# Kernel optimization log

Measured on AMD Instinct MI355X. Metric: run time of the kernel, lower is better.

The kernel has to match this reference:

```python
import jax, jax.numpy as jnp
import numpy as np


def _row_distance(a, b):
    # pairwise cosine similarity between rows of a [N,D] and b [K,D] -> [N,K]
    an = a / (jnp.linalg.norm(a, axis=1, keepdims=True) + 1e-12)
    bn = b / (jnp.linalg.norm(b, axis=1, keepdims=True) + 1e-12)
    return an @ bn.T


def _nearest_context(feature, context):
    sim = _row_distance(feature, context)          # [B, K]
    # distances = -sim; argmin(distances) == argmax(sim)
    min_ind = jnp.argmax(sim, axis=1)              # [B]
    onehot = jax.nn.one_hot(min_ind, context.shape[0], dtype=feature.dtype)  # [B, K]
    rslt = onehot @ jax.lax.stop_gradient(context)  # [B, E] codebook gather
    return rslt, onehot


@jax.custom_vjp
def _vq(feature, context):
    return _nearest_context(feature, context)[0]


def _vq_fwd(feature, context):
    value, ind = _nearest_context(feature, context)
    return value, ind


def _vq_bwd(ind, d_value):
    # straight-through to feature; scatter grads into codebook rows
    return (d_value, ind.T @ d_value)


_vq.defvjp(_vq_fwd, _vq_bwd)


def setup_inputs() -> dict:
    key = jax.random.key(0)
    ks = jax.random.split(key, 6)
    B, FEAT, MID, EMB, K = 8192, 4096, 512, 256, 512
    return {
        "x": jax.random.normal(ks[0], (B, FEAT), dtype=jnp.float32),
        "enc_w1": jax.random.normal(ks[1], (FEAT, MID), dtype=jnp.float32) * 0.02,
        "enc_b1": jnp.zeros((MID,), dtype=jnp.float32),
        "enc_w2": jax.random.normal(ks[2], (MID, EMB), dtype=jnp.float32) * 0.02,
        "enc_b2": jnp.zeros((EMB,), dtype=jnp.float32),
        "emb": jax.random.normal(ks[3], (K, EMB), dtype=jnp.float32) * 0.01,
        "dec_w1": jax.random.normal(ks[4], (EMB, MID), dtype=jnp.float32) * 0.02,
        "dec_b1": jnp.zeros((MID,), dtype=jnp.float32),
        "dec_w2": jax.random.normal(ks[5], (MID, FEAT), dtype=jnp.float32) * 0.02,
        "dec_b2": jnp.zeros((FEAT,), dtype=jnp.float32),
    }


def reference(x, enc_w1, enc_b1, enc_w2, enc_b2, emb, dec_w1, dec_b1, dec_w2, dec_b2):
    # encoder (stand-in for MultiContextEncoder with out_size=(middle_dim, emb_dim))
    h = jax.nn.relu(x @ enc_w1 + enc_b1)           # [B, MID]
    encoded = h @ enc_w2 + enc_b2                  # [B, EMB]
    # vector quantization with straight-through gradient
    vq_feat = _vq(encoded, emb)                    # [B, EMB]
    _, context_ind = _nearest_context(encoded, emb)  # [B, K] one-hot
    # decoder: Dense(middle_dim, relu) -> Dense(feat_dim, relu)
    d = jax.nn.relu(vq_feat @ dec_w1 + dec_b1)     # [B, MID]
    decoded = jax.nn.relu(d @ dec_w2 + dec_b2)     # [B, FEAT]
    return (encoded, vq_feat, context_ind, decoded, emb)
```

## Files before the change

kernel.cpp:

```cpp
#include <hip/hip_runtime.h>

#define BATCH 8192
#define FEAT  4096
#define MID   512
#define EMB   256
#define KCODE 512

typedef _Float16 half8 __attribute__((ext_vector_type(8)));
typedef _Float16 half4v __attribute__((ext_vector_type(4)));
typedef float floatx4 __attribute__((ext_vector_type(4)));

#define SC_X    512.0f
#define SC_W    4096.0f
#define SC_H    512.0f
#define SC_ENC  4096.0f
#define SC_CODE 4096.0f
#define SC_EMB  4096.0f
#define SC_TM   512.0f
#define DS_G1   (1.0f / (SC_X   * SC_W))
#define DS_G2   (1.0f / (SC_H   * SC_W))
#define DS_D1   (1.0f / (SC_EMB * SC_W))
#define DS_D2   (1.0f / (SC_TM  * SC_W))

#define GLD16(gp, lp)                                                          \
    __builtin_amdgcn_global_load_lds(                                          \
        (const __attribute__((address_space(1))) void*)(gp),                   \
        (__attribute__((address_space(3))) void*)(lp), 16, 0, 0)

template<int NT, int AF32>
__global__ __launch_bounds__(256)
void gemm_sk(const float* __restrict__ Af32,
             const _Float16* __restrict__ Ahg, const _Float16* __restrict__ Alg,
             const _Float16* __restrict__ BTh, const _Float16* __restrict__ BTl,
             float aScale,
             float* __restrict__ partOut,
             const float* __restrict__ bias, float descale, int relu,
             float* __restrict__ outF, _Float16* __restrict__ outHi,
             _Float16* __restrict__ outLo, float outScale,
             int M, int N, int K, int lgK, int lgN, int swz)
{
    __shared__ _Float16 AhS[128 * 32];
    __shared__ _Float16 BhS[128 * 32];
    __shared__ _Float16 AlS[NT == 3 ? 128 * 32 : 8];
    __shared__ _Float16 BlS[NT == 3 ? 128 * 32 : 8];

    const int tid  = threadIdx.x;
    const int lane = tid & 63;
    const int wave = tid >> 6;
    const int wm = wave >> 1, wn = wave & 1;
    const int l15  = lane & 15;
    const int quad = lane >> 4;
    const int q8   = quad * 8;

    int bm, bn, ks;
    if (swz) {
        int b = blockIdx.x;
        int mlo = b & 7;
        ks = (b >> 3) & ((1 << lgK) - 1);
        bn = (b >> (3 + lgK)) & ((1 << lgN) - 1);
        bm = ((b >> (3 + lgK + lgN)) << 3) | mlo;
    } else { bm = blockIdx.y; bn = blockIdx.x; ks = 0; }
    const int row0 = bm * 128, col0 = bn * 128;
    const int Kslice = K >> lgK;
    const int k0 = ks * Kslice;

    const int sr4 = tid >> 2;
    const int sc4 = (tid & 3) * 8;
    const size_t aB0 = (size_t)(row0 + sr4) * K + sc4;
    const size_t aB1 = (size_t)(row0 + 64 + sr4) * K + sc4;
    const size_t bB0 = (size_t)(col0 + sr4) * K + sc4;
    const size_t bB1 = (size_t)(col0 + 64 + sr4) * K + sc4;
    const int l0 = tid * 8, l1 = 2048 + tid * 8;

    const int sr2 = tid >> 1;
    const int sk2 = (tid & 1) * 16;
    const size_t aOff2 = (size_t)(row0 + sr2) * K + sk2;
    const int lA = sr2 * 32 + sk2;

    floatx4 acc[4][4] = {};

    for (int kt = 0; kt < Kslice; kt += 32) {
        GLD16(BTh + bB0 + k0 + kt, &BhS[l0]);
        GLD16(BTh + bB1 + k0 + kt, &BhS[l1]);
        if (NT == 3) {
            GLD16(BTl + bB0 + k0 + kt, &BlS[l0]);
            GLD16(BTl + bB1 + k0 + kt, &BlS[l1]);
        }
        if (AF32) {
            const float* p = Af32 + aOff2 + k0 + kt;
            float4 f0 = *(const float4*)(p);
            float4 f1 = *(const float4*)(p + 4);
            float4 f2 = *(const float4*)(p + 8);
            float4 f3 = *(const float4*)(p + 12);
            float fv[16] = {f0.x,f0.y,f0.z,f0.w, f1.x,f1.y,f1.z,f1.w,
                            f2.x,f2.y,f2.z,f2.w, f3.x,f3.y,f3.z,f3.w};
            half8 hv0, hv1, lv0, lv1;
            #pragma unroll
            for (int e = 0; e < 8; ++e) {
                float v = fv[e] * aScale;
                _Float16 h = (_Float16)v;
                hv0[e] = h; lv0[e] = (_Float16)(v - (float)h);
            }
            #pragma unroll
            for (int e = 0; e < 8; ++e) {
                float v = fv[8 + e] * aScale;
                _Float16 h = (_Float16)v;
                hv1[e] = h; lv1[e] = (_Float16)(v - (float)h);
            }
            *(half8*)&AhS[lA] = hv0; *(half8*)&AhS[lA + 8] = hv1;
            if (NT == 3) { *(half8*)&AlS[lA] = lv0; *(half8*)&AlS[lA + 8] = lv1; }
        } else {
            GLD16(Ahg + aB0 + k0 + kt, &AhS[l0]);
            GLD16(Ahg + aB1 + k0 + kt, &AhS[l1]);
            if (NT == 3) {
                GLD16(Alg + aB0 + k0 + kt, &AlS[l0]);
                GLD16(Alg + aB1 + k0 + kt, &AlS[l1]);
            }
        }
        __syncthreads();

        half8 ah[4], al4[4], bh[4], bl4[4];
        #pragma unroll
        for (int i = 0; i < 4; ++i) {
            int ra = (wm * 64 + i * 16 + l15) * 32 + q8;
            int rb = (wn * 64 + i * 16 + l15) * 32 + q8;
            ah[i] = *(const half8*)&AhS[ra];
            bh[i] = *(const half8*)&BhS[rb];
            if (NT == 3) {
                al4[i] = *(const half8*)&AlS[ra];
                bl4[i] = *(const half8*)&BlS[rb];
            }
        }
        #pragma unroll
        for (int i = 0; i < 4; ++i)
            #pragma unroll
            for (int j = 0; j < 4; ++j) {
                acc[i][j] = __builtin_amdgcn_mfma_f32_16x16x32_f16(ah[i], bh[j], acc[i][j], 0, 0, 0);
                if (NT == 3) {
                    acc[i][j] = __builtin_amdgcn_mfma_f32_16x16x32_f16(ah[i],  bl4[j], acc[i][j], 0, 0, 0);
                    acc[i][j] = __builtin_amdgcn_mfma_f32_16x16x32_f16(al4[i], bh[j],  acc[i][j], 0, 0, 0);
                }
            }
        __syncthreads();
    }

    if (partOut) {
        float* po = partOut + (size_t)ks * M * N;
        #pragma unroll
        for (int j = 0; j < 4; ++j) {
            int col = col0 + wn * 64 + j * 16 + l15;
            #pragma unroll
            for (int i = 0; i < 4; ++i)
                #pragma unroll
                for (int t = 0; t < 4; ++t) {
                    int r = row0 + wm * 64 + i * 16 + quad * 4 + t;
                    po[(size_t)r * N + col] = acc[i][j][t];
                }
        }
    } else {
        #pragma unroll
        for (int j = 0; j < 4; ++j) {
            int col = col0 + wn * 64 + j * 16 + l15;
            float bcol = bias ? bias[col] : 0.0f;
            #pragma unroll
            for (int i = 0; i < 4; ++i)
                #pragma unroll
                for (int t = 0; t < 4; ++t) {
                    int r = row0 + wm * 64 + i * 16 + quad * 4 + t;
                    float v = acc[i][j][t] * descale + bcol;
                    if (relu) v = fmaxf(v, 0.0f);
                    size_t o = (size_t)r * N + col;
                    if (outF) outF[o] = v;
                    if (outHi) {
                        float sv = v * outScale;
                        _Float16 h = (_Float16)sv;
                        outHi[o] = h;
                        outLo[o] = (_Float16)(sv - (float)h);
                    }
                }
        }
    }
}

__global__ __launch_bounds__(256)
void reduce_sk(const float* __restrict__ part, int nSlice, int MN, int N,
               const float* __restrict__ bias, float descale, int relu,
               float* __restrict__ outF, _Float16* __restrict__ outHi,
               _Float16* __restrict__ outLo, float outScale)
{
    int i = blockIdx.x * 256 + threadIdx.x;
    if (i * 4 >= MN) return;
    float4 s = ((const float4*)part)[i];
    for (int sl = 1; sl < nSlice; ++sl) {
        float4 p = ((const float4*)(part + (size_t)sl * MN))[i];
        s.x += p.x; s.y += p.y; s.z += p.z; s.w += p.w;
    }
    int col = (i * 4) % N;
    float v[4] = {s.x, s.y, s.z, s.w};
    #pragma unroll
    for (int e = 0; e < 4; ++e) {
        float t = v[e] * descale + (bias ? bias[col + e] : 0.0f);
        if (relu) t = fmaxf(t, 0.0f);
        v[e] = t;
    }
    if (outF) ((float4*)outF)[i] = *(float4*)v;
    if (outHi) {
        half4v hv, lv;
        #pragma unroll
        for (int e = 0; e < 4; ++e) {
            float sv = v[e] * outScale;
            _Float16 h = (_Float16)sv;
            hv[e] = h;
            lv[e] = (_Float16)(sv - (float)h);
        }
        ((half4v*)outHi)[i] = hv;
        ((half4v*)outLo)[i] = lv;
    }
}

__global__ __launch_bounds__(256)
void transpose_split(const float* __restrict__ src, _Float16* __restrict__ hi,
                     _Float16* __restrict__ lo, float scale, int R, int C)
{
    __shared__ float t[32][33];
    int tx = threadIdx.x & 31, ty = threadIdx.x >> 5;
    int r0 = blockIdx.y * 32, c0 = blockIdx.x * 32;
    #pragma unroll
    for (int p = 0; p < 4; ++p) {
        int r = ty + p * 8;
        t[r][tx] = src[(size_t)(r0 + r) * C + c0 + tx];
    }
    __syncthreads();
    #pragma unroll
    for (int p = 0; p < 4; ++p) {
        int oc = ty + p * 8;
        float v = t[tx][oc] * scale;
        _Float16 h = (_Float16)v;
        size_t o = (size_t)(c0 + oc) * R + r0 + tx;
        hi[o] = h;
        lo[o] = (_Float16)(v - (float)h);
    }
}

__global__ __launch_bounds__(256)
void norm_codes(const float* __restrict__ emb, _Float16* __restrict__ cnHi,
                _Float16* __restrict__ cnLo)
{
    int wave = threadIdx.x >> 6;
    int lane = threadIdx.x & 63;
    int c = blockIdx.x * 4 + wave;
    if (c >= KCODE) return;
    const float* er = emb + (size_t)c * EMB;
    float ss = 0.0f;
    #pragma unroll
    for (int k = lane; k < EMB; k += 64) { float v = er[k]; ss += v * v; }
    #pragma unroll
    for (int off = 32; off > 0; off >>= 1) ss += __shfl_down(ss, off, 64);
    ss = __shfl(ss, 0, 64);
    float inv = 1.0f / (sqrtf(ss) + 1e-12f);
    #pragma unroll
    for (int k = lane; k < EMB; k += 64) {
        float v = er[k] * inv * SC_CODE;
        _Float16 h = (_Float16)v;
        cnHi[(size_t)c * EMB + k] = h;
        cnLo[(size_t)c * EMB + k] = (_Float16)(v - (float)h);
    }
}

__global__ __launch_bounds__(256)
void argmax_vq2(const float* __restrict__ part, int MN,
                const float* __restrict__ emb,
                float* __restrict__ onehot, float* __restrict__ vqfeat,
                int* __restrict__ idxOut)
{
    int wave = threadIdx.x >> 6;
    int lane = threadIdx.x & 63;
    int row = blockIdx.x * 4 + wave;
    if (row >= BATCH) return;

    const float* p0 = part + (size_t)row * KCODE;
    const float* p1 = part + (size_t)MN + (size_t)row * KCODE;
    float bestV = -3.402823466e+38f;
    int   bestI = 0;
    #pragma unroll
    for (int c = lane; c < KCODE; c += 64) {
        float v = p0[c] + p1[c];
        if (v > bestV) { bestV = v; bestI = c; }
    }
    #pragma unroll
    for (int off = 32; off > 0; off >>= 1) {
        float ov = __shfl_down(bestV, off, 64);
        int   oi = __shfl_down(bestI, off, 64);
        if (ov > bestV || (ov == bestV && oi < bestI)) { bestV = ov; bestI = oi; }
    }
    bestI = __shfl(bestI, 0, 64);
    if (lane == 0) idxOut[row] = bestI;

    float* oh = onehot + (size_t)row * KCODE;
    #pragma unroll
    for (int c = lane; c < KCODE; c += 64) oh[c] = (c == bestI) ? 1.0f : 0.0f;

    const float* er = emb + (size_t)bestI * EMB;
    float* vr = vqfeat + (size_t)row * EMB;
    #pragma unroll
    for (int c = lane; c < EMB; c += 64) vr[c] = er[c];
}

__global__ __launch_bounds__(256)
void gather_decoded(const float* __restrict__ Dcode, const int* __restrict__ idx,
                    float* __restrict__ out)
{
    int row = blockIdx.x;
    int k = idx[row];
    const float4* src = (const float4*)(Dcode + (size_t)k * FEAT);
    float4* dst = (float4*)(out + (size_t)row * FEAT);
    #pragma unroll
    for (int i = threadIdx.x; i < FEAT / 4; i += 256) dst[i] = src[i];
}

__global__ __launch_bounds__(256)
void copy_f4(const float* __restrict__ src, float* __restrict__ dst, int n4)
{
    int i = blockIdx.x * 256 + threadIdx.x;
    if (i < n4) ((float4*)dst)[i] = ((const float4*)src)[i];
}

extern "C" void kernel_launch(void* const* d_in, const int* in_sizes, int n_in,
                              void* d_out, int out_size, void* d_ws, size_t ws_size,
                              hipStream_t stream)
{
    const float* x      = (const float*)d_in[0];
    const float* enc_w1 = (const float*)d_in[1];
    const float* enc_b1 = (const float*)d_in[2];
    const float* enc_w2 = (const float*)d_in[3];
    const float* enc_b2 = (const float*)d_in[4];
    const float* emb    = (const float*)d_in[5];
    const float* dec_w1 = (const float*)d_in[6];
    const float* dec_b1 = (const float*)d_in[7];
    const float* dec_w2 = (const float*)d_in[8];
    const float* dec_b2 = (const float*)d_in[9];

    float* out = (float*)d_out;
    float* out_encoded = out;
    float* out_vqfeat  = out + (size_t)BATCH * EMB;
    float* out_onehot  = out + (size_t)2 * BATCH * EMB;
    float* out_decoded = out + (size_t)2 * BATCH * EMB + (size_t)BATCH * KCODE;
    float* out_emb     = out_decoded + (size_t)BATCH * FEAT;

    char* w = (char*)d_ws;
    _Float16* w1T_hi = (_Float16*)w;  w += (size_t)FEAT * MID * 2;
    _Float16* w1T_lo = (_Float16*)w;  w += (size_t)FEAT * MID * 2;
    _Float16* w2T_hi = (_Float16*)w;  w += (size_t)MID * EMB * 2;
    _Float16* w2T_lo = (_Float16*)w;  w += (size_t)MID * EMB * 2;
    _Float16* wd1T_hi= (_Float16*)w;  w += (size_t)MID * EMB * 2;
    _Float16* wd1T_lo= (_Float16*)w;  w += (size_t)MID * EMB * 2;
    _Float16* wd2T_hi= (_Float16*)w;  w += (size_t)FEAT * MID * 2;
    _Float16* wd2T_lo= (_Float16*)w;  w += (size_t)FEAT * MID * 2;
    _Float16* h_hi   = (_Float16*)w;  w += (size_t)BATCH * MID * 2;
    _Float16* h_lo   = (_Float16*)w;  w += (size_t)BATCH * MID * 2;
    _Float16* enc_hi = (_Float16*)w;  w += (size_t)BATCH * EMB * 2;
    _Float16* enc_lo = (_Float16*)w;  w += (size_t)BATCH * EMB * 2;
    _Float16* cn_hi  = (_Float16*)w;  w += (size_t)KCODE * EMB * 2;
    _Float16* cn_lo  = (_Float16*)w;  w += (size_t)KCODE * EMB * 2;
    _Float16* tm_hi  = (_Float16*)w;  w += (size_t)KCODE * MID * 2;
    _Float16* tm_lo  = (_Float16*)w;  w += (size_t)KCODE * MID * 2;
    float*    Dc     = (float*)w;     w += (size_t)KCODE * FEAT * 4;
    float*    scr    = (float*)w;     w += (size_t)4 * BATCH * MID * 4;
    int*      idx    = (int*)w;

    transpose_split<<<dim3(MID / 32, FEAT / 32), dim3(256), 0, stream>>>(
        enc_w1, w1T_hi, w1T_lo, SC_W, FEAT, MID);
    transpose_split<<<dim3(EMB / 32, MID / 32), dim3(256), 0, stream>>>(
        enc_w2, w2T_hi, w2T_lo, SC_W, MID, EMB);
    transpose_split<<<dim3(MID / 32, EMB / 32), dim3(256), 0, stream>>>(
        dec_w1, wd1T_hi, wd1T_lo, SC_W, EMB, MID);
    transpose_split<<<dim3(FEAT / 32, MID / 32), dim3(256), 0, stream>>>(
        dec_w2, wd2T_hi, wd2T_lo, SC_W, MID, FEAT);
    norm_codes<<<dim3(KCODE / 4), dim3(256), 0, stream>>>(emb, cn_hi, cn_lo);
    copy_f4<<<dim3((KCODE * EMB / 4 + 255) / 256), dim3(256), 0, stream>>>(
        emb, out_emb, KCODE * EMB / 4);

    gemm_sk<3, 1><<<dim3(1024), dim3(256), 0, stream>>>(
        x, nullptr, nullptr, w1T_hi, w1T_lo, SC_X,
        scr, nullptr, 0.0f, 0, nullptr, nullptr, nullptr, 0.0f,
        BATCH, MID, FEAT, 2, 2, 1);
    reduce_sk<<<dim3(BATCH * MID / 4 / 256), dim3(256), 0, stream>>>(
        scr, 4, BATCH * MID, MID, enc_b1, DS_G1, 1,
        nullptr, h_hi, h_lo, SC_H);

    gemm_sk<3, 0><<<dim3(512), dim3(256), 0, stream>>>(
        nullptr, h_hi, h_lo, w2T_hi, w2T_lo, 0.0f,
        scr, nullptr, 0.0f, 0, nullptr, nullptr, nullptr, 0.0f,
        BATCH, EMB, MID, 2, 1, 1);
    reduce_sk<<<dim3(BATCH * EMB / 4 / 256), dim3(256), 0, stream>>>(
        scr, 4, BATCH * EMB, EMB, enc_b2, DS_G2, 0,
        out_encoded, enc_hi, enc_lo, SC_ENC);

    gemm_sk<3, 0><<<dim3(512), dim3(256), 0, stream>>>(
        nullptr, enc_hi, enc_lo, cn_hi, cn_lo, 0.0f,
        scr, nullptr, 0.0f, 0, nullptr, nullptr, nullptr, 0.0f,
        BATCH, KCODE, EMB, 1, 2, 1);
    argmax_vq2<<<dim3(BATCH / 4), dim3(256), 0, stream>>>(
        scr, BATCH * KCODE, emb, out_onehot, out_vqfeat, idx);

    gemm_sk<1, 1><<<dim3(KCODE / 128, KCODE / 128), dim3(256), 0, stream>>>(
        emb, nullptr, nullptr, wd1T_hi, wd1T_lo, SC_EMB,
        nullptr, dec_b1, DS_D1, 1, nullptr, tm_hi, tm_lo, SC_TM,
        KCODE, MID, EMB, 0, 0, 0);
    gemm_sk<1, 0><<<dim3(FEAT / 128, KCODE / 128), dim3(256), 0, stream>>>(
        nullptr, tm_hi, tm_lo, wd2T_hi, wd2T_lo, 0.0f,
        nullptr, dec_b2, DS_D2, 1, Dc, nullptr, nullptr, 0.0f,
        KCODE, FEAT, MID, 0, 0, 0);

    gather_decoded<<<dim3(BATCH), dim3(256), 0, stream>>>(Dc, idx, out_decoded);
}
```

Measured before the change: 504.3 us.

## Pre-split x into fp16 hi/lo in output buffer and fuse decoded gather into argmax

Converts x into scaled fp16 hi/lo pairs in a separate pass, storing them in the not-yet-written decoded output region, so the first encoder GEMM reads half-precision split operands instead of converting fp32 on the fly. The decoder codebook GEMMs are moved ahead of the encoder so the argmax kernel can copy the decoded rows directly, which removes the separate gather kernel and the index buffer. This adds an extra full read/write pass over x and relies on the decoded output buffer being large enough to hold the split copies before it is overwritten.

```diff
diff --git a/kernel.cpp b/kernel.cpp
--- a/kernel.cpp
+++ b/kernel.cpp
@@ -183,6 +183,28 @@
 }
 
 __global__ __launch_bounds__(256)
+void split_scale(const float* __restrict__ src, _Float16* __restrict__ hi,
+                 _Float16* __restrict__ lo, float scale, int n8)
+{
+    int stride = gridDim.x * 256;
+    for (int i = blockIdx.x * 256 + threadIdx.x; i < n8; i += stride) {
+        const float4* s = (const float4*)src + (size_t)2 * i;
+        float4 a = s[0], b = s[1];
+        float f[8] = {a.x, a.y, a.z, a.w, b.x, b.y, b.z, b.w};
+        half8 hv, lv;
+        #pragma unroll
+        for (int e = 0; e < 8; ++e) {
+            float v = f[e] * scale;
+            _Float16 h = (_Float16)v;
+            hv[e] = h;
+            lv[e] = (_Float16)(v - (float)h);
+        }
+        ((half8*)hi)[i] = hv;
+        ((half8*)lo)[i] = lv;
+    }
+}
+
+__global__ __launch_bounds__(256)
 void reduce_sk(const float* __restrict__ part, int nSlice, int MN, int N,
                const float* __restrict__ bias, float descale, int relu,
                float* __restrict__ outF, _Float16* __restrict__ outHi,
@@ -270,8 +292,9 @@
 __global__ __launch_bounds__(256)
 void argmax_vq2(const float* __restrict__ part, int MN,
                 const float* __restrict__ emb,
+                const float* __restrict__ Dcode,
                 float* __restrict__ onehot, float* __restrict__ vqfeat,
-                int* __restrict__ idxOut)
+                float* __restrict__ decoded)
 {
     int wave = threadIdx.x >> 6;
     int lane = threadIdx.x & 63;
@@ -294,7 +317,6 @@
         if (ov > bestV || (ov == bestV && oi < bestI)) { bestV = ov; bestI = oi; }
     }
     bestI = __shfl(bestI, 0, 64);
-    if (lane == 0) idxOut[row] = bestI;
 
     float* oh = onehot + (size_t)row * KCODE;
     #pragma unroll
@@ -304,18 +326,11 @@
     float* vr = vqfeat + (size_t)row * EMB;
     #pragma unroll
     for (int c = lane; c < EMB; c += 64) vr[c] = er[c];
-}
-
-__global__ __launch_bounds__(256)
-void gather_decoded(const float* __restrict__ Dcode, const int* __restrict__ idx,
-                    float* __restrict__ out)
-{
-    int row = blockIdx.x;
-    int k = idx[row];
-    const float4* src = (const float4*)(Dcode + (size_t)k * FEAT);
-    float4* dst = (float4*)(out + (size_t)row * FEAT);
-    #pragma unroll
-    for (int i = threadIdx.x; i < FEAT / 4; i += 256) dst[i] = src[i];
+
+    const float4* sd = (const float4*)(Dcode + (size_t)bestI * FEAT);
+    float4* dd = (float4*)(decoded + (size_t)row * FEAT);
+    #pragma unroll
+    for (int i = lane; i < FEAT / 4; i += 64) dd[i] = sd[i];
 }
 
 __global__ __launch_bounds__(256)
@@ -346,6 +361,9 @@
     float* out_onehot  = out + (size_t)2 * BATCH * EMB;
     float* out_decoded = out + (size_t)2 * BATCH * EMB + (size_t)BATCH * KCODE;
     float* out_emb     = out_decoded + (size_t)BATCH * FEAT;
+
+    _Float16* x_hi = (_Float16*)out_decoded;
+    _Float16* x_lo = x_hi + (size_t)BATCH * FEAT;
 
     char* w = (char*)d_ws;
     _Float16* w1T_hi = (_Float16*)w;  w += (size_t)FEAT * MID * 2;
@@ -366,7 +384,6 @@
     _Float16* tm_lo  = (_Float16*)w;  w += (size_t)KCODE * MID * 2;
     float*    Dc     = (float*)w;     w += (size_t)KCODE * FEAT * 4;
     float*    scr    = (float*)w;     w += (size_t)4 * BATCH * MID * 4;
-    int*      idx    = (int*)w;
 
     transpose_split<<<dim3(MID / 32, FEAT / 32), dim3(256), 0, stream>>>(
         enc_w1, w1T_hi, w1T_lo, SC_W, FEAT, MID);
@@ -380,29 +397,6 @@
     copy_f4<<<dim3((KCODE * EMB / 4 + 255) / 256), dim3(256), 0, stream>>>(
         emb, out_emb, KCODE * EMB / 4);
 
-    gemm_sk<3, 1><<<dim3(1024), dim3(256), 0, stream>>>(
-        x, nullptr, nullptr, w1T_hi, w1T_lo, SC_X,
-        scr, nullptr, 0.0f, 0, nullptr, nullptr, nullptr, 0.0f,
-        BATCH, MID, FEAT, 2, 2, 1);
-    reduce_sk<<<dim3(BATCH * MID / 4 / 256), dim3(256), 0, stream>>>(
-        scr, 4, BATCH * MID, MID, enc_b1, DS_G1, 1,
-        nullptr, h_hi, h_lo, SC_H);
-
-    gemm_sk<3, 0><<<dim3(512), dim3(256), 0, stream>>>(
-        nullptr, h_hi, h_lo, w2T_hi, w2T_lo, 0.0f,
-        scr, nullptr, 0.0f, 0, nullptr, nullptr, nullptr, 0.0f,
-        BATCH, EMB, MID, 2, 1, 1);
-    reduce_sk<<<dim3(BATCH * EMB / 4 / 256), dim3(256), 0, stream>>>(
-        scr, 4, BATCH * EMB, EMB, enc_b2, DS_G2, 0,
-        out_encoded, enc_hi, enc_lo, SC_ENC);
-
-    gemm_sk<3, 0><<<dim3(512), dim3(256), 0, stream>>>(
-        nullptr, enc_hi, enc_lo, cn_hi, cn_lo, 0.0f,
-        scr, nullptr, 0.0f, 0, nullptr, nullptr, nullptr, 0.0f,
-        BATCH, KCODE, EMB, 1, 2, 1);
-    argmax_vq2<<<dim3(BATCH / 4), dim3(256), 0, stream>>>(
-        scr, BATCH * KCODE, emb, out_onehot, out_vqfeat, idx);
-
     gemm_sk<1, 1><<<dim3(KCODE / 128, KCODE / 128), dim3(256), 0, stream>>>(
         emb, nullptr, nullptr, wd1T_hi, wd1T_lo, SC_EMB,
         nullptr, dec_b1, DS_D1, 1, nullptr, tm_hi, tm_lo, SC_TM,
@@ -412,5 +406,29 @@
         nullptr, dec_b2, DS_D2, 1, Dc, nullptr, nullptr, 0.0f,
         KCODE, FEAT, MID, 0, 0, 0);
 
-    gather_decoded<<<dim3(BATCH), dim3(256), 0, stream>>>(Dc, idx, out_decoded);
-}
+    split_scale<<<dim3(2048), dim3(256), 0, stream>>>(
+        x, x_hi, x_lo, SC_X, BATCH * FEAT / 8);
+
+    gemm_sk<3, 0><<<dim3(1024), dim3(256), 0, stream>>>(
+        nullptr, x_hi, x_lo, w1T_hi, w1T_lo, 0.0f,
+        scr, nullptr, 0.0f, 0, nullptr, nullptr, nullptr, 0.0f,
+        BATCH, MID, FEAT, 2, 2, 1);
+    reduce_sk<<<dim3(BATCH * MID / 4 / 256), dim3(256), 0, stream>>>(
+        scr, 4, BATCH * MID, MID, enc_b1, DS_G1, 1,
+        nullptr, h_hi, h_lo, SC_H);
+
+    gemm_sk<3, 0><<<dim3(512), dim3(256), 0, stream>>>(
+        nullptr, h_hi, h_lo, w2T_hi, w2T_lo, 0.0f,
+        scr, nullptr, 0.0f, 0, nullptr, nullptr, nullptr, 0.0f,
+        BATCH, EMB, MID, 2, 1, 1);
+    reduce_sk<<<dim3(BATCH * EMB / 4 / 256), dim3(256), 0, stream>>>(
+        scr, 4, BATCH * EMB, EMB, enc_b2, DS_G2, 0,
+        out_encoded, enc_hi, enc_lo, SC_ENC);
+
+    gemm_sk<3, 0><<<dim3(512), dim3(256), 0, stream>>>(
+        nullptr, enc_hi, enc_lo, cn_hi, cn_lo, 0.0f,
+        scr, nullptr, 0.0f, 0, nullptr, nullptr, nullptr, 0.0f,
+        BATCH, KCODE, EMB, 1, 2, 1);
+    argmax_vq2<<<dim3(BATCH / 4), dim3(256), 0, stream>>>(
+        scr, BATCH * KCODE, emb, Dc, out_onehot, out_vqfeat, out_decoded);
+}
```

Result: slower. 547.9 us (+8.7%).

## Double-buffer GEMM shared tiles and fuse argmax with decoded gather

Applied to the files above, without the earlier changes.

The GEMM main loop now double-buffers its shared-memory tiles. The next K-step's global-to-LDS loads and fp32 A loads are issued before the MFMA work on the current tile, and the fp32-to-split-half conversion is deferred until after the MFMAs, leaving one barrier per iteration. This is meant to hide global load latency behind MFMA compute, at the cost of doubled LDS use, which may lower occupancy. Separately, the argmax kernel is merged with the decoded-row gather into one block-per-row kernel, removing a launch and the index buffer round trip. To allow this, the decoder-codebook GEMMs are reordered to run before the encoder.

```diff
diff --git a/kernel.cpp b/kernel.cpp
--- a/kernel.cpp
+++ b/kernel.cpp
@@ -39,10 +39,10 @@
              _Float16* __restrict__ outLo, float outScale,
              int M, int N, int K, int lgK, int lgN, int swz)
 {
-    __shared__ _Float16 AhS[128 * 32];
-    __shared__ _Float16 BhS[128 * 32];
-    __shared__ _Float16 AlS[NT == 3 ? 128 * 32 : 8];
-    __shared__ _Float16 BlS[NT == 3 ? 128 * 32 : 8];
+    __shared__ _Float16 AhS[2][128 * 32];
+    __shared__ _Float16 BhS[2][128 * 32];
+    __shared__ _Float16 AlS[NT == 3 ? 2 : 1][NT == 3 ? 128 * 32 : 8];
+    __shared__ _Float16 BlS[NT == 3 ? 2 : 1][NT == 3 ? 128 * 32 : 8];
 
     const int tid  = threadIdx.x;
     const int lane = tid & 63;
@@ -79,56 +79,92 @@
 
     floatx4 acc[4][4] = {};
 
-    for (int kt = 0; kt < Kslice; kt += 32) {
-        GLD16(BTh + bB0 + k0 + kt, &BhS[l0]);
-        GLD16(BTh + bB1 + k0 + kt, &BhS[l1]);
+    auto cvtA = [&](int s, float4 f0, float4 f1, float4 f2, float4 f3) {
+        float fv[16] = {f0.x,f0.y,f0.z,f0.w, f1.x,f1.y,f1.z,f1.w,
+                        f2.x,f2.y,f2.z,f2.w, f3.x,f3.y,f3.z,f3.w};
+        half8 hv0, hv1, lv0, lv1;
+        #pragma unroll
+        for (int e = 0; e < 8; ++e) {
+            float v = fv[e] * aScale;
+            _Float16 h = (_Float16)v;
+            hv0[e] = h; lv0[e] = (_Float16)(v - (float)h);
+        }
+        #pragma unroll
+        for (int e = 0; e < 8; ++e) {
+            float v = fv[8 + e] * aScale;
+            _Float16 h = (_Float16)v;
+            hv1[e] = h; lv1[e] = (_Float16)(v - (float)h);
+        }
+        *(half8*)&AhS[s][lA] = hv0; *(half8*)&AhS[s][lA + 8] = hv1;
         if (NT == 3) {
-            GLD16(BTl + bB0 + k0 + kt, &BlS[l0]);
-            GLD16(BTl + bB1 + k0 + kt, &BlS[l1]);
+            *(half8*)&AlS[s][lA] = lv0; *(half8*)&AlS[s][lA + 8] = lv1;
+        }
+    };
+
+    const int Ksteps = Kslice >> 5;
+
+    {
+        GLD16(BTh + bB0 + k0, &BhS[0][l0]);
+        GLD16(BTh + bB1 + k0, &BhS[0][l1]);
+        if (NT == 3) {
+            GLD16(BTl + bB0 + k0, &BlS[0][l0]);
+            GLD16(BTl + bB1 + k0, &BlS[0][l1]);
         }
         if (AF32) {
-            const float* p = Af32 + aOff2 + k0 + kt;
+            const float* p = Af32 + aOff2 + k0;
             float4 f0 = *(const float4*)(p);
             float4 f1 = *(const float4*)(p + 4);
             float4 f2 = *(const float4*)(p + 8);
             float4 f3 = *(const float4*)(p + 12);
-            float fv[16] = {f0.x,f0.y,f0.z,f0.w, f1.x,f1.y,f1.z,f1.w,
-                            f2.x,f2.y,f2.z,f2.w, f3.x,f3.y,f3.z,f3.w};
-            half8 hv0, hv1, lv0, lv1;
-            #pragma unroll
-            for (int e = 0; e < 8; ++e) {
-                float v = fv[e] * aScale;
-                _Float16 h = (_Float16)v;
-                hv0[e] = h; lv0[e] = (_Float16)(v - (float)h);
+            cvtA(0, f0, f1, f2, f3);
+        } else {
+            GLD16(Ahg + aB0 + k0, &AhS[0][l0]);
+            GLD16(Ahg + aB1 + k0, &AhS[0][l1]);
+            if (NT == 3) {
+                GLD16(Alg + aB0 + k0, &AlS[0][l0]);
+                GLD16(Alg + aB1 + k0, &AlS[0][l1]);
             }
-            #pragma unroll
-            for (int e = 0; e < 8; ++e) {
-                float v = fv[8 + e] * aScale;
-                _Float16 h = (_Float16)v;
-                hv1[e] = h; lv1[e] = (_Float16)(v - (float)h);
+        }
+    }
+    __syncthreads();
+
+    for (int it = 0; it < Ksteps; ++it) {
+        const int cur = it & 1, nxt = cur ^ 1;
+        const bool pf = (it + 1) < Ksteps;
+        float4 f0, f1, f2, f3;
+        if (pf) {
+            const int kk = k0 + (it + 1) * 32;
+            GLD16(BTh + bB0 + kk, &BhS[nxt][l0]);
+            GLD16(BTh + bB1 + kk, &BhS[nxt][l1]);
+            if (NT == 3) {
+                GLD16(BTl + bB0 + kk, &BlS[nxt][l0]);
+                GLD16(BTl + bB1 + kk, &BlS[nxt][l1]);
             }
-            *(half8*)&AhS[lA] = hv0; *(half8*)&AhS[lA + 8] = hv1;
-            if (NT == 3) { *(half8*)&AlS[lA] = lv0; *(half8*)&AlS[lA + 8] = lv1; }
-        } else {
-            GLD16(Ahg + aB0 + k0 + kt, &AhS[l0]);
-            GLD16(Ahg + aB1 + k0 + kt, &AhS[l1]);
-            if (NT == 3) {
-                GLD16(Alg + aB0 + k0 + kt, &AlS[l0]);
-                GLD16(Alg + aB1 + k0 + kt, &AlS[l1]);
+            if (AF32) {
+                const float* p = Af32 + aOff2 + kk;
+                f0 = *(const float4*)(p);
+                f1 = *(const float4*)(p + 4);
+                f2 = *(const float4*)(p + 8);
+                f3 = *(const float4*)(p + 12);
+            } else {
+                GLD16(Ahg + aB0 + kk, &AhS[nxt][l0]);
+                GLD16(Ahg + aB1 + kk, &AhS[nxt][l1]);
+                if (NT == 3) {
+                    GLD16(Alg + aB0 + kk, &AlS[nxt][l0]);
+                    GLD16(Alg + aB1 + kk, &AlS[nxt][l1]);
+                }
             }
         }
-        __syncthreads();
-
         half8 ah[4], al4[4], bh[4], bl4[4];
         #pragma unroll
         for (int i = 0; i < 4; ++i) {
             int ra = (wm * 64 + i * 16 + l15) * 32 + q8;
             int rb = (wn * 64 + i * 16 + l15) * 32 + q8;
-            ah[i] = *(const half8*)&AhS[ra];
-            bh[i] = *(const half8*)&BhS[rb];
+            ah[i] = *(const half8*)&AhS[cur][ra];
+            bh[i] = *(const half8*)&BhS[cur][rb];
             if (NT == 3) {
-                al4[i] = *(const half8*)&AlS[ra];
-                bl4[i] = *(const half8*)&BlS[rb];
+                al4[i] = *(const half8*)&AlS[cur][ra];
+                bl4[i] = *(const half8*)&BlS[cur][rb];
             }
         }
         #pragma unroll
@@ -141,6 +177,7 @@
                     acc[i][j] = __builtin_amdgcn_mfma_f32_16x16x32_f16(al4[i], bh[j],  acc[i][j], 0, 0, 0);
                 }
             }
+        if (AF32 && pf) cvtA(nxt, f0, f1, f2, f3);
         __syncthreads();
     }
 
@@ -268,54 +305,47 @@
 }
 
 __global__ __launch_bounds__(256)
-void argmax_vq2(const float* __restrict__ part, int MN,
+void argmax_vq3(const float* __restrict__ part, int MN,
                 const float* __restrict__ emb,
+                const float* __restrict__ Dcode,
                 float* __restrict__ onehot, float* __restrict__ vqfeat,
-                int* __restrict__ idxOut)
-{
-    int wave = threadIdx.x >> 6;
-    int lane = threadIdx.x & 63;
-    int row = blockIdx.x * 4 + wave;
-    if (row >= BATCH) return;
-
-    const float* p0 = part + (size_t)row * KCODE;
-    const float* p1 = part + (size_t)MN + (size_t)row * KCODE;
-    float bestV = -3.402823466e+38f;
-    int   bestI = 0;
-    #pragma unroll
-    for (int c = lane; c < KCODE; c += 64) {
-        float v = p0[c] + p1[c];
-        if (v > bestV) { bestV = v; bestI = c; }
-    }
-    #pragma unroll
-    for (int off = 32; off > 0; off >>= 1) {
-        float ov = __shfl_down(bestV, off, 64);
-        int   oi = __shfl_down(bestI, off, 64);
-        if (ov > bestV || (ov == bestV && oi < bestI)) { bestV = ov; bestI = oi; }
-    }
-    bestI = __shfl(bestI, 0, 64);
-    if (lane == 0) idxOut[row] = bestI;
+                float* __restrict__ decoded)
+{
+    __shared__ int sBest;
+    const int row = blockIdx.x;
+    const int tid = threadIdx.x;
+
+    if (tid < 64) {
+        const float* p0 = part + (size_t)row * KCODE;
+        const float* p1 = part + (size_t)MN + (size_t)row * KCODE;
+        float bestV = -3.402823466e+38f;
+        int   bestI = 0;
+        #pragma unroll
+        for (int c = tid; c < KCODE; c += 64) {
+            float v = p0[c] + p1[c];
+            if (v > bestV) { bestV = v; bestI = c; }
+        }
+        #pragma unroll
+        for (int off = 32; off > 0; off >>= 1) {
+            float ov = __shfl_down(bestV, off, 64);
+            int   oi = __shfl_down(bestI, off, 64);
+            if (ov > bestV || (ov == bestV && oi < bestI)) { bestV = ov; bestI = oi; }
+        }
+        if (tid == 0) sBest = bestI;
+    }
+    __syncthreads();
+    const int bestI = sBest;
 
     float* oh = onehot + (size_t)row * KCODE;
-    #pragma unroll
-    for (int c = lane; c < KCODE; c += 64) oh[c] = (c == bestI) ? 1.0f : 0.0f;
-
-    const float* er = emb + (size_t)bestI * EMB;
-    float* vr = vqfeat + (size_t)row * EMB;
-    #pragma unroll
-    for (int c = lane; c < EMB; c += 64) vr[c] = er[c];
-}
-
-__global__ __launch_bounds__(256)
-void gather_decoded(const float* __restrict__ Dcode, const int* __restrict__ idx,
-                    float* __restrict__ out)
-{
-    int row = blockIdx.x;
-    int k = idx[row];
-    const float4* src = (const float4*)(Dcode + (size_t)k * FEAT);
-    float4* dst = (float4*)(out + (size_t)row * FEAT);
-    #pragma unroll
-    for (int i = threadIdx.x; i < FEAT / 4; i += 256) dst[i] = src[i];
+    oh[tid]       = (tid       == bestI) ? 1.0f : 0.0f;
+    oh[tid + 256] = (tid + 256 == bestI) ? 1.0f : 0.0f;
+
+    vqfeat[(size_t)row * EMB + tid] = emb[(size_t)bestI * EMB + tid];
+
+    const float4* sd = (const float4*)(Dcode + (size_t)bestI * FEAT);
+    float4* dd = (float4*)(decoded + (size_t)row * FEAT);
+    #pragma unroll
+    for (int i = tid; i < FEAT / 4; i += 256) dd[i] = sd[i];
 }
 
 __global__ __launch_bounds__(256)
@@ -366,7 +396,6 @@
     _Float16* tm_lo  = (_Float16*)w;  w += (size_t)KCODE * MID * 2;
     float*    Dc     = (float*)w;     w += (size_t)KCODE * FEAT * 4;
     float*    scr    = (float*)w;     w += (size_t)4 * BATCH * MID * 4;
-    int*      idx    = (int*)w;
 
     transpose_split<<<dim3(MID / 32, FEAT / 32), dim3(256), 0, stream>>>(
         enc_w1, w1T_hi, w1T_lo, SC_W, FEAT, MID);
@@ -380,29 +409,6 @@
     copy_f4<<<dim3((KCODE * EMB / 4 + 255) / 256), dim3(256), 0, stream>>>(
         emb, out_emb, KCODE * EMB / 4);
 
-    gemm_sk<3, 1><<<dim3(1024), dim3(256), 0, stream>>>(
-        x, nullptr, nullptr, w1T_hi, w1T_lo, SC_X,
-        scr, nullptr, 0.0f, 0, nullptr, nullptr, nullptr, 0.0f,
-        BATCH, MID, FEAT, 2, 2, 1);
-    reduce_sk<<<dim3(BATCH * MID / 4 / 256), dim3(256), 0, stream>>>(
-        scr, 4, BATCH * MID, MID, enc_b1, DS_G1, 1,
-        nullptr, h_hi, h_lo, SC_H);
-
-    gemm_sk<3, 0><<<dim3(512), dim3(256), 0, stream>>>(
-        nullptr, h_hi, h_lo, w2T_hi, w2T_lo, 0.0f,
-        scr, nullptr, 0.0f, 0, nullptr, nullptr, nullptr, 0.0f,
-        BATCH, EMB, MID, 2, 1, 1);
-    reduce_sk<<<dim3(BATCH * EMB / 4 / 256), dim3(256), 0, stream>>>(
-        scr, 4, BATCH * EMB, EMB, enc_b2, DS_G2, 0,
-        out_encoded, enc_hi, enc_lo, SC_ENC);
-
-    gemm_sk<3, 0><<<dim3(512), dim3(256), 0, stream>>>(
-        nullptr, enc_hi, enc_lo, cn_hi, cn_lo, 0.0f,
-        scr, nullptr, 0.0f, 0, nullptr, nullptr, nullptr, 0.0f,
-        BATCH, KCODE, EMB, 1, 2, 1);
-    argmax_vq2<<<dim3(BATCH / 4), dim3(256), 0, stream>>>(
-        scr, BATCH * KCODE, emb, out_onehot, out_vqfeat, idx);
-
     gemm_sk<1, 1><<<dim3(KCODE / 128, KCODE / 128), dim3(256), 0, stream>>>(
         emb, nullptr, nullptr, wd1T_hi, wd1T_lo, SC_EMB,
         nullptr, dec_b1, DS_D1, 1, nullptr, tm_hi, tm_lo, SC_TM,
@@ -412,5 +418,26 @@
         nullptr, dec_b2, DS_D2, 1, Dc, nullptr, nullptr, 0.0f,
         KCODE, FEAT, MID, 0, 0, 0);
 
-    gather_decoded<<<dim3(BATCH), dim3(256), 0, stream>>>(Dc, idx, out_decoded);
-}
+    gemm_sk<3, 1><<<dim3(1024), dim3(256), 0, stream>>>(
+        x, nullptr, nullptr, w1T_hi, w1T_lo, SC_X,
+        scr, nullptr, 0.0f, 0, nullptr, nullptr, nullptr, 0.0f,
+        BATCH, MID, FEAT, 2, 2, 1);
+    reduce_sk<<<dim3(BATCH * MID / 4 / 256), dim3(256), 0, stream>>>(
+        scr, 4, BATCH * MID, MID, enc_b1, DS_G1, 1,
+        nullptr, h_hi, h_lo, SC_H);
+
+    gemm_sk<3, 0><<<dim3(512), dim3(256), 0, stream>>>(
+        nullptr, h_hi, h_lo, w2T_hi, w2T_lo, 0.0f,
+        scr, nullptr, 0.0f, 0, nullptr, nullptr, nullptr, 0.0f,
+        BATCH, EMB, MID, 2, 1, 1);
+    reduce_sk<<<dim3(BATCH * EMB / 4 / 256), dim3(256), 0, stream>>>(
+        scr, 4, BATCH * EMB, EMB, enc_b2, DS_G2, 0,
+        out_encoded, enc_hi, enc_lo, SC_ENC);
+
+    gemm_sk<3, 0><<<dim3(512), dim3(256), 0, stream>>>(
+        nullptr, enc_hi, enc_lo, cn_hi, cn_lo, 0.0f,
+        scr, nullptr, 0.0f, 0, nullptr, nullptr, nullptr, 0.0f,
+        BATCH, KCODE, EMB, 1, 2, 1);
+    argmax_vq3<<<dim3(BATCH), dim3(256), 0, stream>>>(
+        scr, BATCH * KCODE, emb, Dc, out_onehot, out_vqfeat, out_decoded);
+}
```

Result: faster. 492.6 us (-2.3%).
